# Kernel optimization log

Hardware: AMD Instinct MI355X
Metric: run time of the kernel (lower is better)

The kernel has to match this reference:

```python
import jax, jax.numpy as jnp
import numpy as np

EMBED_DIM = 1024
NUM_HEADS = 16
HEAD_DIM = EMBED_DIM // NUM_HEADS
B, N = 8, 1024


def setup_inputs() -> dict:
    key = jax.random.key(0)
    k1, k2, k3, k4, k5, k6 = jax.random.split(key, 6)
    scale = 1.0 / np.sqrt(EMBED_DIM)
    return {
        "x": jax.random.normal(k1, (B, N, EMBED_DIM), dtype=jnp.float32),
        "attn_mask": jax.random.normal(k2, (N, N), dtype=jnp.float32) * 0.1,
        "in_proj_weight": jax.random.normal(k3, (3 * EMBED_DIM, EMBED_DIM), dtype=jnp.float32) * scale,
        "in_proj_bias": jax.random.normal(k4, (3 * EMBED_DIM,), dtype=jnp.float32) * 0.02,
        "out_w": jax.random.normal(k5, (EMBED_DIM, EMBED_DIM), dtype=jnp.float32) * scale,
        "out_b": jax.random.normal(k6, (EMBED_DIM,), dtype=jnp.float32) * 0.02,
    }


def reference(x, attn_mask, in_proj_weight, in_proj_bias, out_w, out_b):
    # x: (B, N, C); fused QKV projection as in forward_direct
    Bn, Nn, C = x.shape
    H, D = NUM_HEADS, HEAD_DIM
    qkv = x @ in_proj_weight.T + in_proj_bias            # (B, N, 3C)
    qkv = qkv.reshape(Bn, Nn, 3, H, D).transpose(2, 0, 3, 1, 4)  # (3, B, H, N, D)
    q, k, v = qkv[0], qkv[1], qkv[2]
    q = q / jnp.sqrt(jnp.asarray(D, dtype=q.dtype))
    attn = jnp.einsum("bhnd,bhmd->bhnm", q, k)           # (B, H, N, N) scores
    attn = attn + attn_mask                              # broadcast over (B, H)
    attn = jax.nn.softmax(attn, axis=-1)
    out = jnp.einsum("bhnm,bhmd->bhnd", attn, v)         # (B, H, N, D)
    out = out.transpose(0, 2, 1, 3).reshape(Bn, Nn, C)   # (B, N, C)
    return out @ out_w.T + out_b
```

## Files before the change

kernel.cpp:

```cpp
#include <hip/hip_runtime.h>


typedef __bf16 bf16x8 __attribute__((ext_vector_type(8)));
typedef float f32x4 __attribute__((ext_vector_type(4)));
typedef unsigned short us4v __attribute__((ext_vector_type(4)));

#define MFMA16 __builtin_amdgcn_mfma_f32_16x16x32_bf16

__device__ __forceinline__ unsigned short f2bf(float f) {
    return __builtin_bit_cast(unsigned short, (__bf16)f);
}

__device__ __forceinline__ us4v cvt4(float4 v) {
    us4v r;
    r.x = f2bf(v.x); r.y = f2bf(v.y); r.z = f2bf(v.z); r.w = f2bf(v.w);
    return r;
}

__device__ __forceinline__ void gl16(const unsigned short* g, unsigned short* l) {
    __builtin_amdgcn_global_load_lds(
        (const __attribute__((address_space(1))) unsigned*)g,
        (__attribute__((address_space(3))) unsigned*)l, 16, 0, 0);
}

__global__ __launch_bounds__(256)
void cvt_bf16(const float* __restrict__ src, unsigned short* __restrict__ dst,
              int n4) {
    const int i = blockIdx.x * 256 + threadIdx.x;
    if (i < n4) {
        float4 v = ((const float4*)src)[i];
        ((us4v*)dst)[i] = cvt4(v);
    }
}

__global__ __launch_bounds__(256, 3)
void qkv_gemm(const unsigned short* __restrict__ xb,
              const unsigned short* __restrict__ wb,
              const float* __restrict__ bias,
              unsigned short* __restrict__ qb, unsigned short* __restrict__ kb,
              unsigned short* __restrict__ vbT)
{
    __shared__ unsigned short lsa[2][128 * 32];
    __shared__ unsigned short lsb[2][128 * 32];
    const int tid  = threadIdx.x;
    const int wave = tid >> 6, lane = tid & 63;
    const int quad = lane >> 4, l15 = lane & 15;
    const int rch = (quad ^ ((l15 >> 1) & 3)) * 8;
    const int m0 = blockIdx.x * 128, n0 = blockIdx.y * 128;
    const int wm = (wave & 1) * 64, wn = (wave >> 1) * 64;

    const int srow = wave * 32 + (lane >> 2);
    const int scol = ((lane & 3) ^ ((lane >> 3) & 3)) * 8;
    const unsigned short* ga = xb + (size_t)(m0 + srow) * 1024 + scol;
    const unsigned short* gb = wb + (size_t)(n0 + srow) * 1024 + scol;
    const int so0 = (wave * 32) * 32;
    const int so1 = (wave * 32 + 16) * 32;

    f32x4 acc[4][4];
#pragma unroll
    for (int i = 0; i < 4; ++i)
#pragma unroll
        for (int j = 0; j < 4; ++j) acc[i][j] = (f32x4){0.f, 0.f, 0.f, 0.f};

    gl16(ga, &lsa[0][so0]);
    gl16(ga + 16 * 1024, &lsa[0][so1]);
    gl16(gb, &lsb[0][so0]);
    gl16(gb + 16 * 1024, &lsb[0][so1]);
    __syncthreads();

    int buf = 0;
    for (int kt = 0; kt < 32; ++kt) {
        if (kt < 31) {
            const int k0 = (kt + 1) * 32;
            gl16(ga + k0, &lsa[buf ^ 1][so0]);
            gl16(ga + 16 * 1024 + k0, &lsa[buf ^ 1][so1]);
            gl16(gb + k0, &lsb[buf ^ 1][so0]);
            gl16(gb + 16 * 1024 + k0, &lsb[buf ^ 1][so1]);
        }
        const unsigned short* pa = lsa[buf];
        const unsigned short* pb = lsb[buf];
        bf16x8 af[4], bfr[4];
#pragma unroll
        for (int i = 0; i < 4; ++i)
            af[i] = *(const bf16x8*)&pa[(wm + i * 16 + l15) * 32 + rch];
#pragma unroll
        for (int j = 0; j < 4; ++j)
            bfr[j] = *(const bf16x8*)&pb[(wn + j * 16 + l15) * 32 + rch];
#pragma unroll
        for (int i = 0; i < 4; ++i)
#pragma unroll
            for (int j = 0; j < 4; ++j)
                acc[i][j] = MFMA16(af[i], bfr[j], acc[i][j], 0, 0, 0);
        __syncthreads();
        buf ^= 1;
    }

    const int which = n0 >> 10;
    if (which == 2) {
#pragma unroll
        for (int j = 0; j < 4; ++j) {
            const int n = n0 + wn + j * 16 + l15;
            const int c = n & 1023;
            const int h = c >> 6, d = c & 63;
            const float bv = bias[n];
#pragma unroll
            for (int i = 0; i < 4; ++i) {
                const int m = m0 + wm + i * 16 + quad * 4;
                const int b = m >> 10, s = m & 1023;
                us4v pk;
#pragma unroll
                for (int r = 0; r < 4; ++r) pk[r] = f2bf(acc[i][j][r] + bv);
                *(us4v*)&vbT[(size_t)((b * 16 + h) * 64 + d) * 1024 + s] = pk;
            }
        }
    } else {
        unsigned short* __restrict__ dst = (which == 0) ? qb : kb;
        const float sc = (which == 0) ? 0.125f : 1.0f;
#pragma unroll
        for (int j = 0; j < 4; ++j) {
            const int n = n0 + wn + j * 16 + l15;
            const int c = n & 1023;
            const int h = c >> 6, d = c & 63;
            const float bv = bias[n];
#pragma unroll
            for (int i = 0; i < 4; ++i)
#pragma unroll
                for (int r = 0; r < 4; ++r) {
                    const int m = m0 + wm + i * 16 + quad * 4 + r;
                    const int b = m >> 10, s = m & 1023;
                    const float v = (acc[i][j][r] + bv) * sc;
                    dst[(size_t)((b * 16 + h) * 1024 + s) * 64 + d] = f2bf(v);
                }
        }
    }
}

__global__ __launch_bounds__(256, 3)
void attn_kernel(const unsigned short* __restrict__ qb,
                 const unsigned short* __restrict__ kb,
                 const unsigned short* __restrict__ vbT,
                 const float* __restrict__ mask,
                 unsigned short* __restrict__ ob)
{
    __shared__ unsigned short lsk[2][2][64 * 32];
    __shared__ unsigned short lsv[2][2][64 * 32];
    __shared__ unsigned short lsp[4][16 * 72];
    const int tid  = threadIdx.x;
    const int wave = tid >> 6, lane = tid & 63;
    const int quad = lane >> 4, l15 = lane & 15;
    const int rch = (quad ^ ((l15 >> 1) & 3)) * 8;
    const int p  = blockIdx.x;
    const int lg = (p & 7) * 256 + (p >> 3);
    const int bh = lg >> 4;
    const int q0 = (lg & 15) * 64;
    const int b = bh >> 4, h = bh & 15;

    const unsigned short* __restrict__ kbase = kb + (size_t)bh * 65536;
    const unsigned short* __restrict__ vtb  = vbT + (size_t)bh * 65536;

    const int scol = ((lane & 3) ^ ((lane >> 3) & 3)) * 8;
    const unsigned short* gk = kbase + (size_t)(wave * 16 + (lane >> 2)) * 64
                                     + scol;
    const unsigned short* gv = vtb + (size_t)(wave * 16 + (lane >> 2)) * 1024
                                   + scol;
    const int so = (wave * 16) * 32;

    bf16x8 bq0, bq1;
    {
        const unsigned short* qrow =
            qb + (size_t)(bh * 1024 + q0 + wave * 16 + l15) * 64;
        bq0 = *(const bf16x8*)(qrow + quad * 8);
        bq1 = *(const bf16x8*)(qrow + 32 + quad * 8);
    }

    float lsum = 0.f;
    f32x4 oacc[4];
#pragma unroll
    for (int nt = 0; nt < 4; ++nt) oacc[nt] = (f32x4){0.f, 0.f, 0.f, 0.f};

    const float* __restrict__ mrow =
        mask + (size_t)(q0 + wave * 16 + l15) * 1024;
    unsigned short* lp = lsp[wave];

    gl16(gk, &lsk[0][0][so]);
    gl16(gk + 32, &lsk[0][1][so]);
    gl16(gv, &lsv[0][0][so]);
    gl16(gv + 32, &lsv[0][1][so]);
    float4 mcur[4];
#pragma unroll
    for (int nt = 0; nt < 4; ++nt)
        mcur[nt] = *(const float4*)&mrow[nt * 16 + quad * 4];
    __syncthreads();

    int buf = 0;
    for (int kt = 0; kt < 16; ++kt) {
        float4 mnext[4];
        if (kt < 15) {
            gl16(gk + (size_t)(kt + 1) * 4096, &lsk[buf ^ 1][0][so]);
            gl16(gk + (size_t)(kt + 1) * 4096 + 32, &lsk[buf ^ 1][1][so]);
            gl16(gv + (size_t)(kt + 1) * 64, &lsv[buf ^ 1][0][so]);
            gl16(gv + (size_t)(kt + 1) * 64 + 32, &lsv[buf ^ 1][1][so]);
#pragma unroll
            for (int nt = 0; nt < 4; ++nt)
                mnext[nt] = *(const float4*)&mrow[(kt + 1) * 64 + nt * 16 + quad * 4];
        }

        const unsigned short* rk0 = lsk[buf][0];
        const unsigned short* rk1 = lsk[buf][1];
        f32x4 s[4];
#pragma unroll
        for (int nt = 0; nt < 4; ++nt) s[nt] = (f32x4){0.f, 0.f, 0.f, 0.f};
        __builtin_amdgcn_s_setprio(1);
#pragma unroll
        for (int nt = 0; nt < 4; ++nt) {
            s[nt] = MFMA16(*(const bf16x8*)&rk0[(nt * 16 + l15) * 32 + rch],
                           bq0, s[nt], 0, 0, 0);
            s[nt] = MFMA16(*(const bf16x8*)&rk1[(nt * 16 + l15) * 32 + rch],
                           bq1, s[nt], 0, 0, 0);
        }
        __builtin_amdgcn_s_setprio(0);

#pragma unroll
        for (int nt = 0; nt < 4; ++nt) {
            us4v pk;
#pragma unroll
            for (int r = 0; r < 4; ++r) {
                const float pe = __expf(s[nt][r] + ((const float*)&mcur[nt])[r]);
                lsum += pe;
                pk[r] = f2bf(pe);
            }
            *(us4v*)&lp[l15 * 72 + nt * 16 + quad * 4] = pk;
        }
        const bf16x8 pb0 = *(const bf16x8*)&lp[l15 * 72 + quad * 8];
        const bf16x8 pb1 = *(const bf16x8*)&lp[l15 * 72 + 32 + quad * 8];

        const unsigned short* rv0 = lsv[buf][0];
        const unsigned short* rv1 = lsv[buf][1];
        __builtin_amdgcn_s_setprio(1);
#pragma unroll
        for (int nt = 0; nt < 4; ++nt) {
            oacc[nt] = MFMA16(*(const bf16x8*)&rv0[(nt * 16 + l15) * 32 + rch],
                              pb0, oacc[nt], 0, 0, 0);
            oacc[nt] = MFMA16(*(const bf16x8*)&rv1[(nt * 16 + l15) * 32 + rch],
                              pb1, oacc[nt], 0, 0, 0);
        }
        __builtin_amdgcn_s_setprio(0);

        __syncthreads();
#pragma unroll
        for (int nt = 0; nt < 4; ++nt) mcur[nt] = mnext[nt];
        buf ^= 1;
    }

    lsum += __shfl_xor(lsum, 16, 64);
    lsum += __shfl_xor(lsum, 32, 64);
    const float inv = 1.0f / lsum;

    unsigned short* orow =
        ob + (size_t)(b * 1024 + q0 + wave * 16 + l15) * 1024 + h * 64;
#pragma unroll
    for (int nt = 0; nt < 4; ++nt) {
        us4v o;
#pragma unroll
        for (int r = 0; r < 4; ++r) o[r] = f2bf(oacc[nt][r] * inv);
        *(us4v*)&orow[nt * 16 + quad * 4] = o;
    }
}

__global__ __launch_bounds__(256, 3)
void out_gemm(const unsigned short* __restrict__ a,
              const unsigned short* __restrict__ wb,
              const float* __restrict__ bias, float* __restrict__ out)
{
    __shared__ unsigned short lsa[2][128 * 32];
    __shared__ unsigned short lsb[2][128 * 32];
    const int tid  = threadIdx.x;
    const int wave = tid >> 6, lane = tid & 63;
    const int quad = lane >> 4, l15 = lane & 15;
    const int rch = (quad ^ ((l15 >> 1) & 3)) * 8;
    const int m0 = blockIdx.x * 128, n0 = blockIdx.y * 128;
    const int wm = (wave & 1) * 64, wn = (wave >> 1) * 64;

    const int srow = wave * 32 + (lane >> 2);
    const int scol = ((lane & 3) ^ ((lane >> 3) & 3)) * 8;
    const unsigned short* ga = a + (size_t)(m0 + srow) * 1024 + scol;
    const unsigned short* gb = wb + (size_t)(n0 + srow) * 1024 + scol;
    const int so0 = (wave * 32) * 32;
    const int so1 = (wave * 32 + 16) * 32;

    f32x4 acc[4][4];
#pragma unroll
    for (int i = 0; i < 4; ++i)
#pragma unroll
        for (int j = 0; j < 4; ++j) acc[i][j] = (f32x4){0.f, 0.f, 0.f, 0.f};

    gl16(ga, &lsa[0][so0]);
    gl16(ga + 16 * 1024, &lsa[0][so1]);
    gl16(gb, &lsb[0][so0]);
    gl16(gb + 16 * 1024, &lsb[0][so1]);
    __syncthreads();

    int buf = 0;
    for (int kt = 0; kt < 32; ++kt) {
        if (kt < 31) {
            const int k0 = (kt + 1) * 32;
            gl16(ga + k0, &lsa[buf ^ 1][so0]);
            gl16(ga + 16 * 1024 + k0, &lsa[buf ^ 1][so1]);
            gl16(gb + k0, &lsb[buf ^ 1][so0]);
            gl16(gb + 16 * 1024 + k0, &lsb[buf ^ 1][so1]);
        }
        const unsigned short* pa = lsa[buf];
        const unsigned short* pb = lsb[buf];
        bf16x8 af[4], bfr[4];
#pragma unroll
        for (int i = 0; i < 4; ++i)
            af[i] = *(const bf16x8*)&pa[(wm + i * 16 + l15) * 32 + rch];
#pragma unroll
        for (int j = 0; j < 4; ++j)
            bfr[j] = *(const bf16x8*)&pb[(wn + j * 16 + l15) * 32 + rch];
#pragma unroll
        for (int i = 0; i < 4; ++i)
#pragma unroll
            for (int j = 0; j < 4; ++j)
                acc[i][j] = MFMA16(af[i], bfr[j], acc[i][j], 0, 0, 0);
        __syncthreads();
        buf ^= 1;
    }

#pragma unroll
    for (int j = 0; j < 4; ++j) {
        const int n = n0 + wn + j * 16 + l15;
        const float bv = bias[n];
#pragma unroll
        for (int i = 0; i < 4; ++i)
#pragma unroll
            for (int r = 0; r < 4; ++r) {
                const int m = m0 + wm + i * 16 + quad * 4 + r;
                out[(size_t)m * 1024 + n] = acc[i][j][r] + bv;
            }
    }
}

extern "C" void kernel_launch(void* const* d_in, const int* in_sizes, int n_in,
                              void* d_out, int out_size, void* d_ws, size_t ws_size,
                              hipStream_t stream) {
    const float* x    = (const float*)d_in[0];
    const float* mask = (const float*)d_in[1];
    const float* win  = (const float*)d_in[2];
    const float* bin  = (const float*)d_in[3];
    const float* wout = (const float*)d_in[4];
    const float* bout = (const float*)d_in[5];
    float* out = (float*)d_out;

    char* ws = (char*)d_ws;
    unsigned short* xb = (unsigned short*)(ws);
    unsigned short* ob = (unsigned short*)(ws);
    unsigned short* qb = (unsigned short*)(ws + (size_t)(16 << 20));
    unsigned short* kb = (unsigned short*)(ws + (size_t)(32 << 20));
    unsigned short* vbT = (unsigned short*)(ws + (size_t)(48 << 20));
    unsigned short* winb  = (unsigned short*)d_out;
    unsigned short* woutb = (unsigned short*)((char*)d_out + (size_t)(6 << 20));

    cvt_bf16<<<dim3(8192), 256, 0, stream>>>(x, xb, 8 * 1024 * 1024 / 4);
    cvt_bf16<<<dim3(3072), 256, 0, stream>>>(win, winb, 3 * 1024 * 1024 / 4);
    cvt_bf16<<<dim3(1024), 256, 0, stream>>>(wout, woutb, 1024 * 1024 / 4);
    qkv_gemm<<<dim3(64, 24), 256, 0, stream>>>(xb, winb, bin, qb, kb, vbT);
    attn_kernel<<<dim3(2048), 256, 0, stream>>>(qb, kb, vbT, mask, ob);
    out_gemm<<<dim3(64, 8), 256, 0, stream>>>(ob, woutb, bout, out);
}
```

Baseline: 288.5 us.

## Process two query groups per wave in attention to reuse K/V tiles

```diff
diff --git a/kernel.cpp b/kernel.cpp
--- a/kernel.cpp
+++ b/kernel.cpp
@@ -144,15 +144,15 @@
 {
     __shared__ unsigned short lsk[2][2][64 * 32];
     __shared__ unsigned short lsv[2][2][64 * 32];
-    __shared__ unsigned short lsp[4][16 * 72];
+    __shared__ unsigned short lsp[4][2][16 * 72];
     const int tid  = threadIdx.x;
     const int wave = tid >> 6, lane = tid & 63;
     const int quad = lane >> 4, l15 = lane & 15;
     const int rch = (quad ^ ((l15 >> 1) & 3)) * 8;
     const int p  = blockIdx.x;
-    const int lg = (p & 7) * 256 + (p >> 3);
-    const int bh = lg >> 4;
-    const int q0 = (lg & 15) * 64;
+    const int lg = (p & 7) * 128 + (p >> 3);
+    const int bh = lg >> 3;
+    const int q0 = (lg & 7) * 128;
     const int b = bh >> 4, h = bh & 15;
 
     const unsigned short* __restrict__ kbase = kb + (size_t)bh * 65536;
@@ -165,105 +165,123 @@
                                    + scol;
     const int so = (wave * 16) * 32;
 
-    bf16x8 bq0, bq1;
-    {
+    bf16x8 bq[2][2];
+#pragma unroll
+    for (int g = 0; g < 2; ++g) {
         const unsigned short* qrow =
-            qb + (size_t)(bh * 1024 + q0 + wave * 16 + l15) * 64;
-        bq0 = *(const bf16x8*)(qrow + quad * 8);
-        bq1 = *(const bf16x8*)(qrow + 32 + quad * 8);
-    }
-
-    float lsum = 0.f;
-    f32x4 oacc[4];
-#pragma unroll
-    for (int nt = 0; nt < 4; ++nt) oacc[nt] = (f32x4){0.f, 0.f, 0.f, 0.f};
-
-    const float* __restrict__ mrow =
-        mask + (size_t)(q0 + wave * 16 + l15) * 1024;
-    unsigned short* lp = lsp[wave];
+            qb + (size_t)(bh * 1024 + q0 + wave * 32 + g * 16 + l15) * 64;
+        bq[g][0] = *(const bf16x8*)(qrow + quad * 8);
+        bq[g][1] = *(const bf16x8*)(qrow + 32 + quad * 8);
+    }
+
+    float lsum[2] = {0.f, 0.f};
+    f32x4 oacc[2][4];
+#pragma unroll
+    for (int g = 0; g < 2; ++g)
+#pragma unroll
+        for (int nt = 0; nt < 4; ++nt) oacc[g][nt] = (f32x4){0.f, 0.f, 0.f, 0.f};
+
+    const float* __restrict__ mrow0 =
+        mask + (size_t)(q0 + wave * 32 + l15) * 1024;
+    const float* __restrict__ mrow1 = mrow0 + 16 * 1024;
 
     gl16(gk, &lsk[0][0][so]);
     gl16(gk + 32, &lsk[0][1][so]);
     gl16(gv, &lsv[0][0][so]);
     gl16(gv + 32, &lsv[0][1][so]);
-    float4 mcur[4];
-#pragma unroll
-    for (int nt = 0; nt < 4; ++nt)
-        mcur[nt] = *(const float4*)&mrow[nt * 16 + quad * 4];
     __syncthreads();
 
     int buf = 0;
     for (int kt = 0; kt < 16; ++kt) {
-        float4 mnext[4];
+        float4 mv[2][4];
+#pragma unroll
+        for (int nt = 0; nt < 4; ++nt) {
+            mv[0][nt] = *(const float4*)&mrow0[kt * 64 + nt * 16 + quad * 4];
+            mv[1][nt] = *(const float4*)&mrow1[kt * 64 + nt * 16 + quad * 4];
+        }
+        __builtin_amdgcn_sched_barrier(0);
         if (kt < 15) {
             gl16(gk + (size_t)(kt + 1) * 4096, &lsk[buf ^ 1][0][so]);
             gl16(gk + (size_t)(kt + 1) * 4096 + 32, &lsk[buf ^ 1][1][so]);
             gl16(gv + (size_t)(kt + 1) * 64, &lsv[buf ^ 1][0][so]);
             gl16(gv + (size_t)(kt + 1) * 64 + 32, &lsv[buf ^ 1][1][so]);
-#pragma unroll
-            for (int nt = 0; nt < 4; ++nt)
-                mnext[nt] = *(const float4*)&mrow[(kt + 1) * 64 + nt * 16 + quad * 4];
         }
 
         const unsigned short* rk0 = lsk[buf][0];
         const unsigned short* rk1 = lsk[buf][1];
-        f32x4 s[4];
-#pragma unroll
-        for (int nt = 0; nt < 4; ++nt) s[nt] = (f32x4){0.f, 0.f, 0.f, 0.f};
+        f32x4 s[2][4];
         __builtin_amdgcn_s_setprio(1);
 #pragma unroll
         for (int nt = 0; nt < 4; ++nt) {
-            s[nt] = MFMA16(*(const bf16x8*)&rk0[(nt * 16 + l15) * 32 + rch],
-                           bq0, s[nt], 0, 0, 0);
-            s[nt] = MFMA16(*(const bf16x8*)&rk1[(nt * 16 + l15) * 32 + rch],
-                           bq1, s[nt], 0, 0, 0);
+            const bf16x8 k0 = *(const bf16x8*)&rk0[(nt * 16 + l15) * 32 + rch];
+            const bf16x8 k1 = *(const bf16x8*)&rk1[(nt * 16 + l15) * 32 + rch];
+            s[0][nt] = MFMA16(k0, bq[0][0], (f32x4){0.f, 0.f, 0.f, 0.f}, 0, 0, 0);
+            s[0][nt] = MFMA16(k1, bq[0][1], s[0][nt], 0, 0, 0);
+            s[1][nt] = MFMA16(k0, bq[1][0], (f32x4){0.f, 0.f, 0.f, 0.f}, 0, 0, 0);
+            s[1][nt] = MFMA16(k1, bq[1][1], s[1][nt], 0, 0, 0);
         }
         __builtin_amdgcn_s_setprio(0);
 
 #pragma unroll
-        for (int nt = 0; nt < 4; ++nt) {
-            us4v pk;
-#pragma unroll
-            for (int r = 0; r < 4; ++r) {
-                const float pe = __expf(s[nt][r] + ((const float*)&mcur[nt])[r]);
-                lsum += pe;
-                pk[r] = f2bf(pe);
+        for (int g = 0; g < 2; ++g) {
+            unsigned short* lp = lsp[wave][g];
+#pragma unroll
+            for (int nt = 0; nt < 4; ++nt) {
+                us4v pk;
+#pragma unroll
+                for (int r = 0; r < 4; ++r) {
+                    const float pe =
+                        __expf(s[g][nt][r] + ((const float*)&mv[g][nt])[r]);
+                    lsum[g] += pe;
+                    pk[r] = f2bf(pe);
+                }
+                *(us4v*)&lp[l15 * 72 + nt * 16 + quad * 4] = pk;
             }
-            *(us4v*)&lp[l15 * 72 + nt * 16 + quad * 4] = pk;
-        }
-        const bf16x8 pb0 = *(const bf16x8*)&lp[l15 * 72 + quad * 8];
-        const bf16x8 pb1 = *(const bf16x8*)&lp[l15 * 72 + 32 + quad * 8];
+        }
+        bf16x8 pb[2][2];
+#pragma unroll
+        for (int g = 0; g < 2; ++g) {
+            const unsigned short* lp = lsp[wave][g];
+            pb[g][0] = *(const bf16x8*)&lp[l15 * 72 + quad * 8];
+            pb[g][1] = *(const bf16x8*)&lp[l15 * 72 + 32 + quad * 8];
+        }
 
         const unsigned short* rv0 = lsv[buf][0];
         const unsigned short* rv1 = lsv[buf][1];
         __builtin_amdgcn_s_setprio(1);
 #pragma unroll
         for (int nt = 0; nt < 4; ++nt) {
-            oacc[nt] = MFMA16(*(const bf16x8*)&rv0[(nt * 16 + l15) * 32 + rch],
-                              pb0, oacc[nt], 0, 0, 0);
-            oacc[nt] = MFMA16(*(const bf16x8*)&rv1[(nt * 16 + l15) * 32 + rch],
-                              pb1, oacc[nt], 0, 0, 0);
+            const bf16x8 v0 = *(const bf16x8*)&rv0[(nt * 16 + l15) * 32 + rch];
+            const bf16x8 v1 = *(const bf16x8*)&rv1[(nt * 16 + l15) * 32 + rch];
+            oacc[0][nt] = MFMA16(v0, pb[0][0], oacc[0][nt], 0, 0, 0);
+            oacc[0][nt] = MFMA16(v1, pb[0][1], oacc[0][nt], 0, 0, 0);
+            oacc[1][nt] = MFMA16(v0, pb[1][0], oacc[1][nt], 0, 0, 0);
+            oacc[1][nt] = MFMA16(v1, pb[1][1], oacc[1][nt], 0, 0, 0);
         }
         __builtin_amdgcn_s_setprio(0);
 
         __syncthreads();
-#pragma unroll
-        for (int nt = 0; nt < 4; ++nt) mcur[nt] = mnext[nt];
         buf ^= 1;
     }
 
-    lsum += __shfl_xor(lsum, 16, 64);
-    lsum += __shfl_xor(lsum, 32, 64);
-    const float inv = 1.0f / lsum;
-
-    unsigned short* orow =
-        ob + (size_t)(b * 1024 + q0 + wave * 16 + l15) * 1024 + h * 64;
-#pragma unroll
-    for (int nt = 0; nt < 4; ++nt) {
-        us4v o;
-#pragma unroll
-        for (int r = 0; r < 4; ++r) o[r] = f2bf(oacc[nt][r] * inv);
-        *(us4v*)&orow[nt * 16 + quad * 4] = o;
+#pragma unroll
+    for (int g = 0; g < 2; ++g) {
+        lsum[g] += __shfl_xor(lsum[g], 16, 64);
+        lsum[g] += __shfl_xor(lsum[g], 32, 64);
+    }
+#pragma unroll
+    for (int g = 0; g < 2; ++g) {
+        const float inv = 1.0f / lsum[g];
+        unsigned short* orow =
+            ob + (size_t)(b * 1024 + q0 + wave * 32 + g * 16 + l15) * 1024
+               + h * 64;
+#pragma unroll
+        for (int nt = 0; nt < 4; ++nt) {
+            us4v o;
+#pragma unroll
+            for (int r = 0; r < 4; ++r) o[r] = f2bf(oacc[g][nt][r] * inv);
+            *(us4v*)&orow[nt * 16 + quad * 4] = o;
+        }
     }
 }
 
@@ -359,12 +377,12 @@
     unsigned short* kb = (unsigned short*)(ws + (size_t)(32 << 20));
     unsigned short* vbT = (unsigned short*)(ws + (size_t)(48 << 20));
     unsigned short* winb  = (unsigned short*)d_out;
-    unsigned short* woutb = (unsigned short*)((char*)d_out + (size_t)(6 << 20));
+    unsigned short* woutb = qb;
 
     cvt_bf16<<<dim3(8192), 256, 0, stream>>>(x, xb, 8 * 1024 * 1024 / 4);
     cvt_bf16<<<dim3(3072), 256, 0, stream>>>(win, winb, 3 * 1024 * 1024 / 4);
+    qkv_gemm<<<dim3(64, 24), 256, 0, stream>>>(xb, winb, bin, qb, kb, vbT);
+    attn_kernel<<<dim3(1024), 256, 0, stream>>>(qb, kb, vbT, mask, ob);
     cvt_bf16<<<dim3(1024), 256, 0, stream>>>(wout, woutb, 1024 * 1024 / 4);
-    qkv_gemm<<<dim3(64, 24), 256, 0, stream>>>(xb, winb, bin, qb, kb, vbT);
-    attn_kernel<<<dim3(2048), 256, 0, stream>>>(qb, kb, vbT, mask, ob);
     out_gemm<<<dim3(64, 8), 256, 0, stream>>>(ob, woutb, bout, out);
 }
```

Result: faster. 280.3 us (-2.8%).
